# Optimization experiments

Measured on AMD Instinct MI355X. Metric: run time of the kernel, lower is better.

Reference implementation:

```python
import jax, jax.numpy as jnp
import numpy as np


def setup_inputs() -> dict:
    key = jax.random.key(0)
    ks = jax.random.split(key, 7)
    C = 64
    s = 1.0 / np.sqrt(C)  # torch Linear default init scale (approx, kaiming-uniform-ish)
    return {
        "x": jax.random.normal(ks[0], (8, C, 64, 64), dtype=jnp.float32),
        "Wq": jax.random.normal(ks[1], (C, C), dtype=jnp.float32) * s,
        "bq": jax.random.normal(ks[2], (C,), dtype=jnp.float32) * s,
        "Wk": jax.random.normal(ks[3], (C, C), dtype=jnp.float32) * s,
        "bk": jax.random.normal(ks[4], (C,), dtype=jnp.float32) * s,
        "Wv": jax.random.normal(ks[5], (C, C), dtype=jnp.float32) * s,
        "bv": jax.random.normal(ks[6], (C,), dtype=jnp.float32) * s,
    }


def reference(x, Wq, bq, Wk, bk, Wv, bv):
    B, C, H, W = x.shape
    # [B, C, H, W] -> [B, N, C] with N = H*W (tokens over spatial positions)
    t = x.reshape(B, C, H * W).transpose(0, 2, 1)
    q = t @ Wq.T + bq  # [B, N, C]
    k = t @ Wk.T + bk
    v = t @ Wv.T + bv
    scale = 1.0 / jnp.sqrt(jnp.asarray(C, dtype=t.dtype))
    scores = jnp.einsum("bnc,bmc->bnm", q, k) * scale  # [B, N, N]
    attn = jax.nn.softmax(scores, axis=-1)
    out = jnp.einsum("bnm,bmc->bnc", attn, v)  # [B, N, C]
    return out.transpose(0, 2, 1).reshape(B, C, H, W)
```

## Files before the change

kernel.cpp:

```cpp
#include <hip/hip_runtime.h>
#include <stdint.h>

typedef __attribute__((ext_vector_type(8))) short short8;
typedef __attribute__((ext_vector_type(4))) short short4v;
typedef __attribute__((ext_vector_type(4))) float f32x4;
typedef __attribute__((ext_vector_type(16))) float f32x16;
typedef __attribute__((ext_vector_type(4))) int i32x4;

#define B_ 8
#define C_ 64
#define N_ 4096

__device__ __forceinline__ unsigned short f2bf(float f) {
  unsigned int u = __float_as_uint(f);
  u = (u + 0x7fffu + ((u >> 16) & 1u)) >> 16;
  return (unsigned short)u;
}
__device__ __forceinline__ int pk2t(float lo, float hi2) {
  return (int)__builtin_amdgcn_perm(__float_as_uint(hi2), __float_as_uint(lo),
                                    0x07060302u);
}


#define MFMA32(A, B, C) __builtin_amdgcn_mfma_f32_32x32x16_bf16(A, B, C, 0, 0, 0)

__global__ __launch_bounds__(256) void qkv_mfma(
    const float* __restrict__ x,
    const float* __restrict__ Wq, const float* __restrict__ bq,
    const float* __restrict__ Wk, const float* __restrict__ bk,
    const float* __restrict__ Wv, const float* __restrict__ bv,
    unsigned short* __restrict__ qo, unsigned short* __restrict__ kf,
    unsigned short* __restrict__ vf) {
  const int w = threadIdx.x >> 6;
  const int lane = threadIdx.x & 63;
  const int q31 = lane & 31;
  const int hi = lane >> 5;
  const int m = blockIdx.y;
  const int b = blockIdx.z;
  const int tok = blockIdx.x * 128 + w * 32 + q31;

  const f32x16 Z0 = {0.f,0.f,0.f,0.f,0.f,0.f,0.f,0.f,0.f,0.f,0.f,0.f,0.f,0.f,0.f,0.f};
  const float sc = 0.18033688011112042f;

  short8 xb[4];
  const float* xcol = x + (size_t)b * C_ * N_ + tok;
#pragma unroll
  for (int ks = 0; ks < 4; ++ks) {
    short8 t;
#pragma unroll
    for (int jj = 0; jj < 8; ++jj)
      t[jj] = (short)f2bf(xcol[(size_t)(ks * 16 + hi * 8 + jj) * N_]);
    xb[ks] = t;
  }

  const float* W = (m == 0) ? Wq : (m == 1) ? Wk : Wv;
  const float* bi = (m == 0) ? bq : (m == 1) ? bk : bv;
#pragma unroll
  for (int ot = 0; ot < 2; ++ot) {
    const float* wrow = W + (ot * 32 + q31) * 64 + hi * 8;
    short8 wa0, wa1, wa2, wa3;
    {
      short8 t;
#pragma unroll
      for (int jj = 0; jj < 8; ++jj) t[jj] = (short)f2bf(wrow[jj]);
      wa0 = t;
#pragma unroll
      for (int jj = 0; jj < 8; ++jj) t[jj] = (short)f2bf(wrow[16 + jj]);
      wa1 = t;
#pragma unroll
      for (int jj = 0; jj < 8; ++jj) t[jj] = (short)f2bf(wrow[32 + jj]);
      wa2 = t;
#pragma unroll
      for (int jj = 0; jj < 8; ++jj) t[jj] = (short)f2bf(wrow[48 + jj]);
      wa3 = t;
    }
    f32x16 acc = MFMA32(wa0, xb[0], Z0);
    acc = MFMA32(wa1, xb[1], acc);
    acc = MFMA32(wa2, xb[2], acc);
    acc = MFMA32(wa3, xb[3], acc);

    if (m == 0) {
      unsigned short* dst = qo + ((size_t)b * N_ + tok) * 64;
#pragma unroll
      for (int g = 0; g < 4; ++g) {
        const int ob = 8 * g + 4 * hi + 32 * ot;
        short4v res;
#pragma unroll
        for (int i = 0; i < 4; ++i)
          res[i] = (short)f2bf((acc[4 * g + i] + bi[ob + i]) * sc);
        *(short4v*)(dst + ob) = res;
      }
    } else if (m == 1) {
      const int T = tok >> 5;
      unsigned short* kb_ = kf + (size_t)b * N_ * 64;
#pragma unroll
      for (int g = 0; g < 4; ++g) {
        const int ob = 8 * g + 4 * hi + 32 * ot;
        const int f = ob >> 4;
        const int l = (tok & 31) + 32 * ((ob >> 3) & 1);
        short4v res;
#pragma unroll
        for (int i = 0; i < 4; ++i)
          res[i] = (short)f2bf(acc[4 * g + i] + bi[ob + i]);
        *(short4v*)(kb_ + ((size_t)T * 4 + f) * 512 + l * 8 + (ob & 7)) = res;
      }
    } else {
      const int piece = (tok >> 5) * 4 + ot * 2 + ((tok >> 4) & 1);
      const int jv = (tok & 3) | (((tok >> 3) & 1) << 2);
      const int lb32 = 32 * ((tok >> 2) & 1);
      unsigned short* vbase = vf + (size_t)b * N_ * 64 + (size_t)piece * 512 + jv;
#pragma unroll
      for (int r = 0; r < 16; ++r) {
        const int o31 = (r & 3) + 8 * (r >> 2) + 4 * hi;
        vbase[(o31 + lb32) * 8] = f2bf(acc[r] + bi[o31 + 32 * ot]);
      }
    }
  }
}

#define GLDS(SRC, DST) \
  __builtin_amdgcn_global_load_lds( \
      (const __attribute__((address_space(1))) unsigned int*)(SRC), \
      (__attribute__((address_space(3))) unsigned int*)(DST), 16, 0, 0)

#define STAGE2(SET, TA, TB) { \
  GLDS(kb + (size_t)(TA) * 2048 + w * 512 + lane * 8, &lK[SET][0][w * 512]); \
  GLDS(vb + (size_t)(TA) * 2048 + w * 512 + lane * 8, &lV[SET][0][w * 512]); \
  GLDS(kb + (size_t)(TB) * 2048 + w * 512 + lane * 8, &lK[SET][1][w * 512]); \
  GLDS(vb + (size_t)(TB) * 2048 + w * 512 + lane * 8, &lV[SET][1][w * 512]); \
}

#define LDSK(KF, SET, P) { \
  const unsigned short* kr_ = &lK[SET][P][lane * 8]; \
  KF##0 = *(const short8*)(kr_);        KF##1 = *(const short8*)(kr_ + 512); \
  KF##2 = *(const short8*)(kr_ + 1024); KF##3 = *(const short8*)(kr_ + 1536); }

#define LDSV(VF, SET, P) { \
  const unsigned short* vr_ = &lV[SET][P][lane * 8]; \
  VF##0 = *(const short8*)(vr_);        VF##1 = *(const short8*)(vr_ + 512); \
  VF##2 = *(const short8*)(vr_ + 1024); VF##3 = *(const short8*)(vr_ + 1536); }

#define S_PHASE(S, KF) do { \
  S = MFMA32(KF##0, qf0, Z0); \
  S = MFMA32(KF##1, qf1, S); \
  S = MFMA32(KF##2, qf2, S); \
  S = MFMA32(KF##3, qf3, S); \
} while (0)

#define SMPV(S, VF) do { \
  _Pragma("unroll") \
  for (int r_ = 0; r_ < 16; ++r_) S[r_] = __builtin_amdgcn_exp2f(S[r_]); \
  const short8 P0 = __builtin_bit_cast(short8, \
      (i32x4){pk2t(S[0], S[1]), pk2t(S[2], S[3]), pk2t(S[4], S[5]), pk2t(S[6], S[7])}); \
  const short8 P1 = __builtin_bit_cast(short8, \
      (i32x4){pk2t(S[8], S[9]), pk2t(S[10], S[11]), pk2t(S[12], S[13]), pk2t(S[14], S[15])}); \
  ls = MFMA32(ONES, P0, ls); ls = MFMA32(ONES, P1, ls); \
  o0 = MFMA32(VF##0, P0, o0); o0 = MFMA32(VF##1, P1, o0); \
  o1 = MFMA32(VF##2, P0, o1); o1 = MFMA32(VF##3, P1, o1); \
} while (0)

__global__ __launch_bounds__(256, 4) void flash_attn2(
    const unsigned short* __restrict__ q,
    const unsigned short* __restrict__ kf,
    const unsigned short* __restrict__ vf,
    float* __restrict__ out,
    unsigned short* __restrict__ po, float* __restrict__ pl,
    int nsplit, int tiles) {
  const int b = blockIdx.x & 7;
  const int j = blockIdx.x >> 3;
  const int w = threadIdx.x >> 6;
  const int item = j * 4 + w;
  const int qb = item & 127;
  const int split = item >> 7;
  const int lane = threadIdx.x & 63;
  const int q31 = lane & 31;
  const int hi = lane >> 5;

  __shared__ __align__(16) unsigned short lK[2][2][2048];
  __shared__ __align__(16) unsigned short lV[2][2][2048];

  const unsigned short* qp = q + ((size_t)b * N_ + qb * 32 + q31) * 64 + hi * 8;
  short8 qf0 = *(const short8*)(qp);
  short8 qf1 = *(const short8*)(qp + 16);
  short8 qf2 = *(const short8*)(qp + 32);
  short8 qf3 = *(const short8*)(qp + 48);

  const short one_ = (short)0x3F80;
  const short8 ONES = (short8){one_, one_, one_, one_, one_, one_, one_, one_};
  const f32x16 Z0 = {0.f,0.f,0.f,0.f,0.f,0.f,0.f,0.f,0.f,0.f,0.f,0.f,0.f,0.f,0.f,0.f};

  const unsigned short* kb = kf + (size_t)b * N_ * 64;
  const unsigned short* vb = vf + (size_t)b * N_ * 64;

  f32x16 o0 = Z0, o1 = Z0, ls = Z0;
  f32x16 s;

  short8 kA0, kA1, kA2, kA3;
  short8 vA0, vA1, vA2, vA3;

  const int t0 = split * tiles, t1 = t0 + tiles;
  STAGE2(0, t0, t0 + 1);
  __syncthreads();
  for (int t = t0; t < t1; t += 2) {
    const int cur = ((t - t0) >> 1) & 1;
    if (t + 2 < t1) STAGE2(cur ^ 1, t + 2, t + 3);
    LDSK(kA, cur, 0);
    LDSV(vA, cur, 0);
    S_PHASE(s, kA);
    SMPV(s, vA);
    LDSK(kA, cur, 1);
    LDSV(vA, cur, 1);
    S_PHASE(s, kA);
    SMPV(s, vA);
    __syncthreads();
  }

  const float lt_ = ls[0];
  const int n_ = qb * 32 + q31;
  if (nsplit == 1) {
    const float inv = 1.f / lt_;
    float* ob = out + (size_t)b * 64 * N_ + n_;
#pragma unroll
    for (int r_ = 0; r_ < 16; ++r_) {
      const int cl = (r_ & 3) + 8 * (r_ >> 2) + 4 * hi;
      ob[(size_t)cl * N_] = o0[r_] * inv;
      ob[(size_t)(cl + 32) * N_] = o1[r_] * inv;
    }
  } else {
    unsigned short* pr = po + ((size_t)(split * B_ + b) * 64) * N_ + n_;
#pragma unroll
    for (int r_ = 0; r_ < 16; ++r_) {
      const int cl = (r_ & 3) + 8 * (r_ >> 2) + 4 * hi;
      pr[(size_t)cl * N_] = f2bf(o0[r_]);
      pr[(size_t)(cl + 32) * N_] = f2bf(o1[r_]);
    }
    if (hi == 0) pl[(size_t)(split * B_ + b) * N_ + n_] = lt_;
  }
}

template <int NS>
__global__ __launch_bounds__(256) void combine_k(
    const unsigned short* __restrict__ po, const float* __restrict__ pl,
    float* __restrict__ out) {
  const int n2 = (blockIdx.x * 256 + threadIdx.x) * 2;
  const int c0 = blockIdx.y * 8;
  const int b = blockIdx.z;
  const size_t sb = (size_t)B_ * N_;

  float l0 = 0.f, l1 = 0.f;
#pragma unroll
  for (int s = 0; s < NS; ++s) {
    const float2 pv = *(const float2*)(pl + s * sb + (size_t)b * N_ + n2);
    l0 += pv.x; l1 += pv.y;
  }
  const float inv0 = 1.f / l0, inv1 = 1.f / l1;

#pragma unroll
  for (int cc = 0; cc < 8; ++cc) {
    float a0 = 0.f, a1 = 0.f;
#pragma unroll
    for (int s = 0; s < NS; ++s) {
      const unsigned v = *(const unsigned*)(
          po + ((size_t)(s * B_ + b) * 64 + c0 + cc) * N_ + n2);
      a0 += __uint_as_float(v << 16);
      a1 += __uint_as_float(v & 0xFFFF0000u);
    }
    float2 r;
    r.x = a0 * inv0; r.y = a1 * inv1;
    *(float2*)(out + ((size_t)b * 64 + c0 + cc) * N_ + n2) = r;
  }
}

extern "C" void kernel_launch(void* const* d_in, const int* in_sizes, int n_in,
                              void* d_out, int out_size, void* d_ws, size_t ws_size,
                              hipStream_t stream) {
  const float* x  = (const float*)d_in[0];
  const float* Wq = (const float*)d_in[1];
  const float* bq = (const float*)d_in[2];
  const float* Wk = (const float*)d_in[3];
  const float* bk = (const float*)d_in[4];
  const float* Wv = (const float*)d_in[5];
  const float* bv = (const float*)d_in[6];
  float* out = (float*)d_out;

  unsigned short* qws = (unsigned short*)d_ws;
  unsigned short* kws = qws + (size_t)B_ * N_ * 64;
  unsigned short* vws = kws + (size_t)B_ * N_ * 64;

  const size_t qkv_bytes = (size_t)3 * B_ * N_ * 64 * 2;
  const size_t per_split = (size_t)B_ * N_ * 64 * 2 + (size_t)B_ * N_ * 4;

  int S = 1;
  if (ws_size >= qkv_bytes + 4 * per_split) S = 4;
  else if (ws_size >= qkv_bytes + 2 * per_split) S = 2;

  unsigned short* po = (unsigned short*)((char*)d_ws + qkv_bytes);
  float* pl = (float*)(po + (size_t)S * B_ * N_ * 64);

  qkv_mfma<<<dim3(N_ / 128, 3, B_), 256, 0, stream>>>(
      x, Wq, bq, Wk, bk, Wv, bv, qws, kws, vws);

  flash_attn2<<<256 * S, 256, 0, stream>>>(qws, kws, vws, out, po, pl, S, 128 / S);

  if (S == 4)      combine_k<4><<<dim3(N_ / 512, 8, B_), 256, 0, stream>>>(po, pl, out);
  else if (S == 2) combine_k<2><<<dim3(N_ / 512, 8, B_), 256, 0, stream>>>(po, pl, out);
}
```

Before: 64.64 us.

## Process two query blocks per wave to reuse K/V fragments

Each wave now handles 64 query rows as two 32-row blocks. The K and V fragments it reads from LDS are reused for both sets of MFMAs, which halves LDS traffic and global K/V staging per query. To fit the extra accumulators, the grid shrinks by half and launch bounds drop to 2 blocks per SM. The risks are lower occupancy and fewer blocks in flight, which could leave CUs underused.

```diff
diff --git a/kernel.cpp b/kernel.cpp
--- a/kernel.cpp
+++ b/kernel.cpp
@@ -140,26 +140,26 @@
   VF##0 = *(const short8*)(vr_);        VF##1 = *(const short8*)(vr_ + 512); \
   VF##2 = *(const short8*)(vr_ + 1024); VF##3 = *(const short8*)(vr_ + 1536); }
 
-#define S_PHASE(S, KF) do { \
-  S = MFMA32(KF##0, qf0, Z0); \
-  S = MFMA32(KF##1, qf1, S); \
-  S = MFMA32(KF##2, qf2, S); \
-  S = MFMA32(KF##3, qf3, S); \
+#define S_PHASE(S, KF, QF) do { \
+  S = MFMA32(KF##0, QF##0, Z0); \
+  S = MFMA32(KF##1, QF##1, S); \
+  S = MFMA32(KF##2, QF##2, S); \
+  S = MFMA32(KF##3, QF##3, S); \
 } while (0)
 
-#define SMPV(S, VF) do { \
+#define SMPV(S, VF, O0, O1, LS) do { \
   _Pragma("unroll") \
   for (int r_ = 0; r_ < 16; ++r_) S[r_] = __builtin_amdgcn_exp2f(S[r_]); \
   const short8 P0 = __builtin_bit_cast(short8, \
       (i32x4){pk2t(S[0], S[1]), pk2t(S[2], S[3]), pk2t(S[4], S[5]), pk2t(S[6], S[7])}); \
   const short8 P1 = __builtin_bit_cast(short8, \
       (i32x4){pk2t(S[8], S[9]), pk2t(S[10], S[11]), pk2t(S[12], S[13]), pk2t(S[14], S[15])}); \
-  ls = MFMA32(ONES, P0, ls); ls = MFMA32(ONES, P1, ls); \
-  o0 = MFMA32(VF##0, P0, o0); o0 = MFMA32(VF##1, P1, o0); \
-  o1 = MFMA32(VF##2, P0, o1); o1 = MFMA32(VF##3, P1, o1); \
+  LS = MFMA32(ONES, P0, LS); LS = MFMA32(ONES, P1, LS); \
+  O0 = MFMA32(VF##0, P0, O0); O0 = MFMA32(VF##1, P1, O0); \
+  O1 = MFMA32(VF##2, P0, O1); O1 = MFMA32(VF##3, P1, O1); \
 } while (0)
 
-__global__ __launch_bounds__(256, 4) void flash_attn2(
+__global__ __launch_bounds__(256, 2) void flash_attn2(
     const unsigned short* __restrict__ q,
     const unsigned short* __restrict__ kf,
     const unsigned short* __restrict__ vf,
@@ -170,8 +170,8 @@
   const int j = blockIdx.x >> 3;
   const int w = threadIdx.x >> 6;
   const int item = j * 4 + w;
-  const int qb = item & 127;
-  const int split = item >> 7;
+  const int p = item & 63;
+  const int split = item >> 6;
   const int lane = threadIdx.x & 63;
   const int q31 = lane & 31;
   const int hi = lane >> 5;
@@ -179,11 +179,16 @@
   __shared__ __align__(16) unsigned short lK[2][2][2048];
   __shared__ __align__(16) unsigned short lV[2][2][2048];
 
-  const unsigned short* qp = q + ((size_t)b * N_ + qb * 32 + q31) * 64 + hi * 8;
-  short8 qf0 = *(const short8*)(qp);
-  short8 qf1 = *(const short8*)(qp + 16);
-  short8 qf2 = *(const short8*)(qp + 32);
-  short8 qf3 = *(const short8*)(qp + 48);
+  const unsigned short* qpA = q + ((size_t)b * N_ + p * 64 + q31) * 64 + hi * 8;
+  short8 qfA0 = *(const short8*)(qpA);
+  short8 qfA1 = *(const short8*)(qpA + 16);
+  short8 qfA2 = *(const short8*)(qpA + 32);
+  short8 qfA3 = *(const short8*)(qpA + 48);
+  const unsigned short* qpB = qpA + (size_t)32 * 64;
+  short8 qfB0 = *(const short8*)(qpB);
+  short8 qfB1 = *(const short8*)(qpB + 16);
+  short8 qfB2 = *(const short8*)(qpB + 32);
+  short8 qfB3 = *(const short8*)(qpB + 48);
 
   const short one_ = (short)0x3F80;
   const short8 ONES = (short8){one_, one_, one_, one_, one_, one_, one_, one_};
@@ -192,7 +197,8 @@
   const unsigned short* kb = kf + (size_t)b * N_ * 64;
   const unsigned short* vb = vf + (size_t)b * N_ * 64;
 
-  f32x16 o0 = Z0, o1 = Z0, ls = Z0;
+  f32x16 o0A = Z0, o1A = Z0, lsA = Z0;
+  f32x16 o0B = Z0, o1B = Z0, lsB = Z0;
   f32x16 s;
 
   short8 kA0, kA1, kA2, kA3;
@@ -204,37 +210,45 @@
   for (int t = t0; t < t1; t += 2) {
     const int cur = ((t - t0) >> 1) & 1;
     if (t + 2 < t1) STAGE2(cur ^ 1, t + 2, t + 3);
-    LDSK(kA, cur, 0);
-    LDSV(vA, cur, 0);
-    S_PHASE(s, kA);
-    SMPV(s, vA);
-    LDSK(kA, cur, 1);
-    LDSV(vA, cur, 1);
-    S_PHASE(s, kA);
-    SMPV(s, vA);
+#pragma unroll
+    for (int P = 0; P < 2; ++P) {
+      LDSK(kA, cur, P);
+      LDSV(vA, cur, P);
+      S_PHASE(s, kA, qfA);
+      SMPV(s, vA, o0A, o1A, lsA);
+      S_PHASE(s, kA, qfB);
+      SMPV(s, vA, o0B, o1B, lsB);
+    }
     __syncthreads();
   }
 
-  const float lt_ = ls[0];
-  const int n_ = qb * 32 + q31;
+  const int nA = p * 64 + q31;
+  const int nB = nA + 32;
   if (nsplit == 1) {
-    const float inv = 1.f / lt_;
-    float* ob = out + (size_t)b * 64 * N_ + n_;
+    const float invA = 1.f / lsA[0], invB = 1.f / lsB[0];
+    float* ob = out + (size_t)b * 64 * N_;
 #pragma unroll
     for (int r_ = 0; r_ < 16; ++r_) {
       const int cl = (r_ & 3) + 8 * (r_ >> 2) + 4 * hi;
-      ob[(size_t)cl * N_] = o0[r_] * inv;
-      ob[(size_t)(cl + 32) * N_] = o1[r_] * inv;
+      ob[(size_t)cl * N_ + nA] = o0A[r_] * invA;
+      ob[(size_t)(cl + 32) * N_ + nA] = o1A[r_] * invA;
+      ob[(size_t)cl * N_ + nB] = o0B[r_] * invB;
+      ob[(size_t)(cl + 32) * N_ + nB] = o1B[r_] * invB;
     }
   } else {
-    unsigned short* pr = po + ((size_t)(split * B_ + b) * 64) * N_ + n_;
+    unsigned short* pr = po + ((size_t)(split * B_ + b) * 64) * N_;
 #pragma unroll
     for (int r_ = 0; r_ < 16; ++r_) {
       const int cl = (r_ & 3) + 8 * (r_ >> 2) + 4 * hi;
-      pr[(size_t)cl * N_] = f2bf(o0[r_]);
-      pr[(size_t)(cl + 32) * N_] = f2bf(o1[r_]);
-    }
-    if (hi == 0) pl[(size_t)(split * B_ + b) * N_ + n_] = lt_;
+      pr[(size_t)cl * N_ + nA] = f2bf(o0A[r_]);
+      pr[(size_t)(cl + 32) * N_ + nA] = f2bf(o1A[r_]);
+      pr[(size_t)cl * N_ + nB] = f2bf(o0B[r_]);
+      pr[(size_t)(cl + 32) * N_ + nB] = f2bf(o1B[r_]);
+    }
+    if (hi == 0) {
+      pl[(size_t)(split * B_ + b) * N_ + nA] = lsA[0];
+      pl[(size_t)(split * B_ + b) * N_ + nB] = lsB[0];
+    }
   }
 }
 
@@ -300,7 +314,7 @@
   qkv_mfma<<<dim3(N_ / 128, 3, B_), 256, 0, stream>>>(
       x, Wq, bq, Wk, bk, Wv, bv, qws, kws, vws);
 
-  flash_attn2<<<256 * S, 256, 0, stream>>>(qws, kws, vws, out, po, pl, S, 128 / S);
+  flash_attn2<<<128 * S, 256, 0, stream>>>(qws, kws, vws, out, po, pl, S, 128 / S);
 
   if (S == 4)      combine_k<4><<<dim3(N_ / 512, 8, B_), 256, 0, stream>>>(po, pl, out);
   else if (S == 2) combine_k<2><<<dim3(N_ / 512, 8, B_), 256, 0, stream>>>(po, pl, out);
```

Measured after the change: 62.88 us. 1.03x faster.
